# Kernel optimization log

Hardware: AMD Instinct MI355X
Metric: run time of the kernel (lower is better)

The kernel has to match this reference:

```python
import jax, jax.numpy as jnp
import numpy as np

B, P, D, H = 4, 2048, 768, 12
DFF = 4 * D
EPS = 1e-3  # Keras LayerNormalization default epsilon
SURVIVAL_PROB = 0.9  # inference-mode droppath scaling


def setup_inputs() -> dict:
    key = jax.random.key(0)
    ks = jax.random.split(key, 4)
    s = 0.02
    return {
        "x": jax.random.normal(ks[0], (B, P, D), dtype=jnp.float32),
        "ln1_g": jnp.ones((D,), jnp.float32),
        "ln1_b": jnp.zeros((D,), jnp.float32),
        "w_qkv": jax.random.normal(ks[1], (D, 3 * D), jnp.float32) * s,
        "b_qkv": jnp.zeros((3 * D,), jnp.float32),
        "ln2_g": jnp.ones((D,), jnp.float32),
        "ln2_b": jnp.zeros((D,), jnp.float32),
        "w1": jax.random.normal(ks[2], (D, DFF), jnp.float32) * s,
        "b1": jnp.zeros((DFF,), jnp.float32),
        "w2": jax.random.normal(ks[3], (DFF, D), jnp.float32) * s,
        "b2": jnp.zeros((D,), jnp.float32),
    }


def _layernorm(x, g, b):
    mu = jnp.mean(x, axis=-1, keepdims=True)
    var = jnp.mean(jnp.square(x - mu), axis=-1, keepdims=True)
    return (x - mu) * jax.lax.rsqrt(var + EPS) * g + b


def _block(x, ln1_g, ln1_b, w_qkv, b_qkv, ln2_g, ln2_b, w1, b1, w2, b2):
    # --- pre-norm self-attention ---
    h = _layernorm(x, ln1_g, ln1_b)
    qkv = h @ w_qkv + b_qkv                      # [B,P,3D]
    q, k, v = jnp.split(qkv, 3, axis=-1)
    hd = D // H
    to_heads = lambda t: t.reshape(B, P, H, hd).transpose(0, 2, 1, 3)  # b h p c
    q, k, v = to_heads(q), to_heads(k), to_heads(v)
    scale = jnp.sqrt(jnp.float32(D / H))
    scores = jnp.einsum('bhqc,bhkc->bhqk', q, k) / scale
    attn = jax.nn.softmax(scores, axis=-1)
    o = jnp.einsum('bhqk,bhkc->bhqc', attn, v)
    o = o.transpose(0, 2, 1, 3).reshape(B, P, D)
    x = o * SURVIVAL_PROB + x
    # --- pre-norm MLP ---
    h = _layernorm(x, ln2_g, ln2_b)
    h = jax.nn.gelu(h @ w1 + b1, approximate=False)
    h = h @ w2 + b2
    return h * SURVIVAL_PROB + x


def reference(x, ln1_g, ln1_b, w_qkv, b_qkv, ln2_g, ln2_b, w1, b1, w2, b2):
    return _block(x, ln1_g, ln1_b, w_qkv, b_qkv, ln2_g, ln2_b, w1, b1, w2, b2)
```

## Files before the change

kernel.cpp:

```cpp
#include <hip/hip_runtime.h>
#include <hip/hip_bf16.h>
#include <math.h>

#define B_ 4
#define P_ 2048
#define D_ 768
#define H_ 12

typedef __attribute__((ext_vector_type(8))) short bf16x8;
typedef __attribute__((ext_vector_type(4))) float f32x4;

static __device__ __forceinline__ short f2bf(float f) {
  union { float f; unsigned u; } z; z.f = f;
  unsigned r = z.u + 0x7fffu + ((z.u >> 16) & 1u);
  return (short)(r >> 16);
}

static __device__ __forceinline__ float bf2f(short s) {
  union { unsigned u; float f; } z;
  z.u = ((unsigned)(unsigned short)s) << 16;
  return z.f;
}

static __device__ __forceinline__ void gll16(const void* g, void* l) {
  __builtin_amdgcn_global_load_lds(
      (const __attribute__((address_space(1))) void*)g,
      (__attribute__((address_space(3))) void*)l, 16, 0, 0);
}

static __device__ __forceinline__ int vswz(int d) {
  return ((d & 7) ^ ((d >> 3) & 7)) << 3;
}

__global__ __launch_bounds__(256) void tcvt_kernel(const float* __restrict__ in,
                                                   short* __restrict__ out, int K, int N) {
  __shared__ float t[32][33];
  int k0 = blockIdx.x * 32, n0 = blockIdx.y * 32;
  int tx = threadIdx.x & 31, ty = threadIdx.x >> 5;
#pragma unroll
  for (int i = 0; i < 4; ++i)
    t[ty + 8 * i][tx] = in[(size_t)(k0 + ty + 8 * i) * N + n0 + tx];
  __syncthreads();
#pragma unroll
  for (int i = 0; i < 4; ++i)
    out[(size_t)(n0 + ty + 8 * i) * K + k0 + tx] = f2bf(t[tx][ty + 8 * i]);
}

__global__ __launch_bounds__(256) void ln_kernel(const float* __restrict__ in,
                                                 const float* __restrict__ g,
                                                 const float* __restrict__ be,
                                                 short* __restrict__ out) {
  int row = blockIdx.x, tid = threadIdx.x;
  const float* xr = in + (size_t)row * D_;
  float v0 = xr[tid], v1 = xr[tid + 256], v2 = xr[tid + 512];
  float s = v0 + v1 + v2;
  float ss = v0 * v0 + v1 * v1 + v2 * v2;
#pragma unroll
  for (int d = 1; d < 64; d <<= 1) {
    s += __shfl_xor(s, d, 64);
    ss += __shfl_xor(ss, d, 64);
  }
  __shared__ float red[8];
  int w = tid >> 6;
  if ((tid & 63) == 0) { red[w] = s; red[4 + w] = ss; }
  __syncthreads();
  s = red[0] + red[1] + red[2] + red[3];
  ss = red[4] + red[5] + red[6] + red[7];
  float mu = s * (1.0f / D_);
  float rstd = rsqrtf(ss * (1.0f / D_) - mu * mu + 1e-3f);
  short* orow = out + (size_t)row * D_;
  orow[tid]       = f2bf((v0 - mu) * rstd * g[tid]       + be[tid]);
  orow[tid + 256] = f2bf((v1 - mu) * rstd * g[tid + 256] + be[tid + 256]);
  orow[tid + 512] = f2bf((v2 - mu) * rstd * g[tid + 512] + be[tid + 512]);
}

template <int EPI>
__global__ __launch_bounds__(256, 3) void gemm128(
    const short* __restrict__ A, const short* __restrict__ Bt,
    const float* __restrict__ bias, short* __restrict__ out_bf,
    float* __restrict__ out_f, const float* __restrict__ resid,
    int M, int N, int K) {
  alignas(16) __shared__ short a_lds[2][128 * 32];
  alignas(16) __shared__ short b_lds[2][128 * 32];
  const int tid = threadIdx.x;
  const int wv = tid >> 6, lane = tid & 63;
  const int wm = wv >> 1, wn = wv & 1;
  const int g = lane >> 4, r = lane & 15;
  const int m0 = blockIdx.x * 128, n0 = blockIdx.y * 128;
  const int srow = lane >> 2, sseg = lane & 3;
  f32x4 acc[4][4] = {};
  const short* aptr = A + (size_t)(m0 + wv * 16 + srow) * K + sseg * 8;
  const short* bptr = Bt + (size_t)(n0 + wv * 16 + srow) * K + sseg * 8;
  const int aoff = (wv * 16) * 32;

  gll16(aptr, &a_lds[0][aoff]);
  gll16(aptr + (size_t)64 * K, &a_lds[0][aoff + 64 * 32]);
  gll16(bptr, &b_lds[0][aoff]);
  gll16(bptr + (size_t)64 * K, &b_lds[0][aoff + 64 * 32]);
  __syncthreads();

  const int nt = K / 32;
  int cur = 0;
  for (int t = 0; t < nt; ++t) {
    if (t + 1 < nt) {
      const int k0 = (t + 1) * 32;
      const int nb = cur ^ 1;
      gll16(aptr + k0, &a_lds[nb][aoff]);
      gll16(aptr + k0 + (size_t)64 * K, &a_lds[nb][aoff + 64 * 32]);
      gll16(bptr + k0, &b_lds[nb][aoff]);
      gll16(bptr + k0 + (size_t)64 * K, &b_lds[nb][aoff + 64 * 32]);
    }
    bf16x8 af[4], bfr[4];
#pragma unroll
    for (int i = 0; i < 4; ++i)
      af[i] = *reinterpret_cast<const bf16x8*>(&a_lds[cur][(wm * 64 + i * 16 + r) * 32 + g * 8]);
#pragma unroll
    for (int i = 0; i < 4; ++i)
      bfr[i] = *reinterpret_cast<const bf16x8*>(&b_lds[cur][(wn * 64 + i * 16 + r) * 32 + g * 8]);
#pragma unroll
    for (int i = 0; i < 4; ++i)
#pragma unroll
      for (int jn = 0; jn < 4; ++jn)
        acc[i][jn] = __builtin_amdgcn_mfma_f32_16x16x32_bf16(af[i], bfr[jn], acc[i][jn], 0, 0, 0);
    __syncthreads();
    cur ^= 1;
  }
#pragma unroll
  for (int i = 0; i < 4; ++i) {
#pragma unroll
    for (int jn = 0; jn < 4; ++jn) {
      int col = n0 + wn * 64 + jn * 16 + r;
      float bb = bias[col];
#pragma unroll
      for (int jj = 0; jj < 4; ++jj) {
        int row = m0 + wm * 64 + i * 16 + g * 4 + jj;
        float v = acc[i][jn][jj] + bb;
        size_t idx = (size_t)row * N + col;
        if (EPI == 0) {
          out_bf[idx] = f2bf(v);
        } else if (EPI == 1) {
          v = 0.5f * v * (1.0f + erff(v * 0.70710678118654752f));
          out_bf[idx] = f2bf(v);
        } else {
          out_f[idx] = v * 0.9f + resid[idx];
        }
      }
    }
  }
}

__global__ __launch_bounds__(256, 3) void attn_kernel(const short* __restrict__ qkv,
                                                      const float* __restrict__ x,
                                                      float* __restrict__ x2) {
  alignas(16) __shared__ short k_lds[64 * 72];
  alignas(16) __shared__ short vt_lds[64 * 64];
  alignas(16) __shared__ short p_lds[4][32 * 72];
  const int tid = threadIdx.x, wv = tid >> 6, lane = tid & 63;
  const int g = lane >> 4, r = lane & 15;
  const int b = blockIdx.y / H_, h = blockIdx.y % H_;
  const int TD = 3 * D_;
  const int qrow0 = blockIdx.x * 128 + wv * 32;
  bf16x8 qf[2][2];
#pragma unroll
  for (int mf = 0; mf < 2; ++mf)
#pragma unroll
    for (int kb = 0; kb < 2; ++kb) {
      bf16x8 q = *reinterpret_cast<const bf16x8*>(
          qkv + (size_t)(b * P_ + qrow0 + mf * 16 + r) * TD + h * 64 + kb * 32 + g * 8);
#pragma unroll
      for (int e = 0; e < 8; ++e) q[e] = f2bf(bf2f(q[e]) * 0.125f);
      qf[mf][kb] = q;
    }
  f32x4 acc[2][4] = {};
  float m_run[2], l_run[2];
#pragma unroll
  for (int mf = 0; mf < 2; ++mf) { m_run[mf] = -1e30f; l_run[mf] = 0.0f; }
  const int lrow = tid >> 2, lseg = tid & 3;
  short* p_w = &p_lds[wv][0];
  const int bcast = 20 * g;
  for (int kc = 0; kc < P_; kc += 64) {
    const short* src = qkv + (size_t)(b * P_ + kc + lrow) * TD + D_ + h * 64 + lseg * 16;
    bf16x8 kv0 = *reinterpret_cast<const bf16x8*>(src);
    bf16x8 kv1 = *reinterpret_cast<const bf16x8*>(src + 8);
    bf16x8 vv0 = *reinterpret_cast<const bf16x8*>(src + D_);
    bf16x8 vv1 = *reinterpret_cast<const bf16x8*>(src + D_ + 8);
    __syncthreads();
    *reinterpret_cast<bf16x8*>(&k_lds[lrow * 72 + lseg * 16]) = kv0;
    *reinterpret_cast<bf16x8*>(&k_lds[lrow * 72 + lseg * 16 + 8]) = kv1;
#pragma unroll
    for (int j = 0; j < 8; ++j) {
      int d0 = lseg * 16 + j, d1 = d0 + 8;
      vt_lds[d0 * 64 + (lrow ^ vswz(d0))] = vv0[j];
      vt_lds[d1 * 64 + (lrow ^ vswz(d1))] = vv1[j];
    }
    __syncthreads();
    f32x4 st[2][4];
#pragma unroll
    for (int cf = 0; cf < 4; ++cf) {
      bf16x8 kf0 = *reinterpret_cast<const bf16x8*>(&k_lds[(cf * 16 + r) * 72 + g * 8]);
      bf16x8 kf1 = *reinterpret_cast<const bf16x8*>(&k_lds[(cf * 16 + r) * 72 + 32 + g * 8]);
#pragma unroll
      for (int mf = 0; mf < 2; ++mf) {
        f32x4 s = {};
        s = __builtin_amdgcn_mfma_f32_16x16x32_bf16(kf0, qf[mf][0], s, 0, 0, 0);
        s = __builtin_amdgcn_mfma_f32_16x16x32_bf16(kf1, qf[mf][1], s, 0, 0, 0);
        st[mf][cf] = s;
      }
    }
#pragma unroll
    for (int mf = 0; mf < 2; ++mf) {
      float mx = st[mf][0][0];
#pragma unroll
      for (int cf = 0; cf < 4; ++cf)
#pragma unroll
        for (int j = 0; j < 4; ++j) mx = fmaxf(mx, st[mf][cf][j]);
      mx = fmaxf(mx, __shfl_xor(mx, 16, 64));
      mx = fmaxf(mx, __shfl_xor(mx, 32, 64));
      if (!__all(mx - m_run[mf] <= 8.0f)) {
        float mn = fmaxf(m_run[mf], mx);
        float corr = __expf(m_run[mf] - mn);
        m_run[mf] = mn;
        l_run[mf] *= corr;
        float cb0 = __shfl(corr, bcast + 0, 64);
        float cb1 = __shfl(corr, bcast + 1, 64);
        float cb2 = __shfl(corr, bcast + 2, 64);
        float cb3 = __shfl(corr, bcast + 3, 64);
#pragma unroll
        for (int cf = 0; cf < 4; ++cf) {
          acc[mf][cf][0] *= cb0; acc[mf][cf][1] *= cb1;
          acc[mf][cf][2] *= cb2; acc[mf][cf][3] *= cb3;
        }
      }
      float mn = m_run[mf];
      float p[4][4];
      float ls = 0.0f;
#pragma unroll
      for (int cf = 0; cf < 4; ++cf)
#pragma unroll
        for (int j = 0; j < 4; ++j) {
          float pv = __expf(st[mf][cf][j] - mn);
          p[cf][j] = pv;
          ls += pv;
        }
      ls += __shfl_xor(ls, 16, 64);
      ls += __shfl_xor(ls, 32, 64);
      l_run[mf] += ls;
      short* prow = &p_w[(mf * 16 + r) * 72];
#pragma unroll
      for (int cf = 0; cf < 4; ++cf) {
        __hip_bfloat162 lo = __float22bfloat162_rn(make_float2(p[cf][0], p[cf][1]));
        __hip_bfloat162 hi = __float22bfloat162_rn(make_float2(p[cf][2], p[cf][3]));
        union { __hip_bfloat162 h2; unsigned u; } c0, c1;
        c0.h2 = lo; c1.h2 = hi;
        *reinterpret_cast<uint2*>(&prow[cf * 16 + 4 * g]) = make_uint2(c0.u, c1.u);
      }
    }
    bf16x8 vf[4][2];
#pragma unroll
    for (int cf = 0; cf < 4; ++cf) {
      int d = cf * 16 + r;
      int sw = vswz(d);
      vf[cf][0] = *reinterpret_cast<const bf16x8*>(&vt_lds[d * 64 + ((g * 8) ^ sw)]);
      vf[cf][1] = *reinterpret_cast<const bf16x8*>(&vt_lds[d * 64 + ((32 + g * 8) ^ sw)]);
    }
#pragma unroll
    for (int mf = 0; mf < 2; ++mf) {
      bf16x8 pf0 = *reinterpret_cast<const bf16x8*>(&p_w[(mf * 16 + r) * 72 + g * 8]);
      bf16x8 pf1 = *reinterpret_cast<const bf16x8*>(&p_w[(mf * 16 + r) * 72 + 32 + g * 8]);
#pragma unroll
      for (int cf = 0; cf < 4; ++cf) {
        acc[mf][cf] = __builtin_amdgcn_mfma_f32_16x16x32_bf16(pf0, vf[cf][0], acc[mf][cf], 0, 0, 0);
        acc[mf][cf] = __builtin_amdgcn_mfma_f32_16x16x32_bf16(pf1, vf[cf][1], acc[mf][cf], 0, 0, 0);
      }
    }
  }
#pragma unroll
  for (int mf = 0; mf < 2; ++mf) {
    float lb0 = 0.9f / __shfl(l_run[mf], bcast + 0, 64);
    float lb1 = 0.9f / __shfl(l_run[mf], bcast + 1, 64);
    float lb2 = 0.9f / __shfl(l_run[mf], bcast + 2, 64);
    float lb3 = 0.9f / __shfl(l_run[mf], bcast + 3, 64);
    float lb[4] = {lb0, lb1, lb2, lb3};
#pragma unroll
    for (int cf = 0; cf < 4; ++cf) {
      int col = h * 64 + cf * 16 + r;
#pragma unroll
      for (int j = 0; j < 4; ++j) {
        int row = qrow0 + mf * 16 + g * 4 + j;
        size_t idx = (size_t)(b * P_ + row) * D_ + col;
        x2[idx] = acc[mf][cf][j] * lb[j] + x[idx];
      }
    }
  }
}

extern "C" void kernel_launch(void* const* d_in, const int* in_sizes, int n_in,
                              void* d_out, int out_size, void* d_ws, size_t ws_size,
                              hipStream_t stream) {
  const float* x     = (const float*)d_in[0];
  const float* ln1_g = (const float*)d_in[1];
  const float* ln1_b = (const float*)d_in[2];
  const float* w_qkv = (const float*)d_in[3];
  const float* b_qkv = (const float*)d_in[4];
  const float* ln2_g = (const float*)d_in[5];
  const float* ln2_b = (const float*)d_in[6];
  const float* w1    = (const float*)d_in[7];
  const float* b1    = (const float*)d_in[8];
  const float* w2    = (const float*)d_in[9];
  const float* b2    = (const float*)d_in[10];
  float* out = (float*)d_out;
  char* ws = (char*)d_ws;

  short* wqkv_t = (short*)(ws);
  short* w1_t   = (short*)(ws + 3538944);
  short* w2_t   = (short*)(ws + 8257536);
  short* h_bf   = (short*)(ws + 12976128);
  short* qkv_bf = (short*)(ws + 25559040);
  short* a1_bf  = qkv_bf;

  const int R = B_ * P_;

  { dim3 g2(768 / 32, 2304 / 32);  tcvt_kernel<<<g2, 256, 0, stream>>>(w_qkv, wqkv_t, 768, 2304); }
  { dim3 g2(768 / 32, 3072 / 32);  tcvt_kernel<<<g2, 256, 0, stream>>>(w1, w1_t, 768, 3072); }
  { dim3 g2(3072 / 32, 768 / 32);  tcvt_kernel<<<g2, 256, 0, stream>>>(w2, w2_t, 3072, 768); }

  ln_kernel<<<R, 256, 0, stream>>>(x, ln1_g, ln1_b, h_bf);

  {
    dim3 grid(R / 128, 2304 / 128);
    gemm128<0><<<grid, 256, 0, stream>>>(h_bf, wqkv_t, b_qkv, qkv_bf, nullptr, nullptr,
                                         R, 2304, 768);
  }
  {
    dim3 grid(P_ / 128, B_ * H_);
    attn_kernel<<<grid, 256, 0, stream>>>(qkv_bf, x, out);
  }
  ln_kernel<<<R, 256, 0, stream>>>(out, ln2_g, ln2_b, h_bf);
  {
    dim3 grid(R / 128, 3072 / 128);
    gemm128<1><<<grid, 256, 0, stream>>>(h_bf, w1_t, b1, a1_bf, nullptr, nullptr,
                                         R, 3072, 768);
  }
  {
    dim3 grid(R / 128, 768 / 128);
    gemm128<2><<<grid, 256, 0, stream>>>(a1_bf, w2_t, b2, nullptr, out, out,
                                         R, 768, 3072);
  }
}
```

Before: 400.3 us.

## Widen attention KV tiles to 128, prefetch next tile into registers, swizzle GEMM LDS

```diff
diff --git a/kernel.cpp b/kernel.cpp
--- a/kernel.cpp
+++ b/kernel.cpp
@@ -26,10 +26,6 @@
   __builtin_amdgcn_global_load_lds(
       (const __attribute__((address_space(1))) void*)g,
       (__attribute__((address_space(3))) void*)l, 16, 0, 0);
-}
-
-static __device__ __forceinline__ int vswz(int d) {
-  return ((d & 7) ^ ((d >> 3) & 7)) << 3;
 }
 
 __global__ __launch_bounds__(256) void tcvt_kernel(const float* __restrict__ in,
@@ -89,8 +85,9 @@
   const int m0 = blockIdx.x * 128, n0 = blockIdx.y * 128;
   const int srow = lane >> 2, sseg = lane & 3;
   f32x4 acc[4][4] = {};
-  const short* aptr = A + (size_t)(m0 + wv * 16 + srow) * K + sseg * 8;
-  const short* bptr = Bt + (size_t)(n0 + wv * 16 + srow) * K + sseg * 8;
+  const int sw_seg = sseg ^ (srow & 3);
+  const short* aptr = A + (size_t)(m0 + wv * 16 + srow) * K + sw_seg * 8;
+  const short* bptr = Bt + (size_t)(n0 + wv * 16 + srow) * K + sw_seg * 8;
   const int aoff = (wv * 16) * 32;
 
   gll16(aptr, &a_lds[0][aoff]);
@@ -113,10 +110,12 @@
     bf16x8 af[4], bfr[4];
 #pragma unroll
     for (int i = 0; i < 4; ++i)
-      af[i] = *reinterpret_cast<const bf16x8*>(&a_lds[cur][(wm * 64 + i * 16 + r) * 32 + g * 8]);
+      af[i] = *reinterpret_cast<const bf16x8*>(
+          &a_lds[cur][(wm * 64 + i * 16 + r) * 32 + ((g ^ (r & 3)) * 8)]);
 #pragma unroll
     for (int i = 0; i < 4; ++i)
-      bfr[i] = *reinterpret_cast<const bf16x8*>(&b_lds[cur][(wn * 64 + i * 16 + r) * 32 + g * 8]);
+      bfr[i] = *reinterpret_cast<const bf16x8*>(
+          &b_lds[cur][(wn * 64 + i * 16 + r) * 32 + ((g ^ (r & 3)) * 8)]);
 #pragma unroll
     for (int i = 0; i < 4; ++i)
 #pragma unroll
@@ -149,12 +148,12 @@
   }
 }
 
-__global__ __launch_bounds__(256, 3) void attn_kernel(const short* __restrict__ qkv,
+__global__ __launch_bounds__(256, 2) void attn_kernel(const short* __restrict__ qkv,
                                                       const float* __restrict__ x,
                                                       float* __restrict__ x2) {
-  alignas(16) __shared__ short k_lds[64 * 72];
-  alignas(16) __shared__ short vt_lds[64 * 64];
-  alignas(16) __shared__ short p_lds[4][32 * 72];
+  alignas(16) __shared__ short k_lds[128 * 64];
+  alignas(16) __shared__ short vt_lds[64 * 128];
+  alignas(16) __shared__ short p_lds[4][32 * 128];
   const int tid = threadIdx.x, wv = tid >> 6, lane = tid & 63;
   const int g = lane >> 4, r = lane & 15;
   const int b = blockIdx.y / H_, h = blockIdx.y % H_;
@@ -175,30 +174,45 @@
   float m_run[2], l_run[2];
 #pragma unroll
   for (int mf = 0; mf < 2; ++mf) { m_run[mf] = -1e30f; l_run[mf] = 0.0f; }
-  const int lrow = tid >> 2, lseg = tid & 3;
-  short* p_w = &p_lds[wv][0];
+
+  const int krow = tid >> 1, dhalf = tid & 1;
+  const short* kv0src = qkv + (size_t)(b * P_ + krow) * TD + D_ + h * 64 + dhalf * 32;
+  char* p_w = (char*)&p_lds[wv][0];
   const int bcast = 20 * g;
-  for (int kc = 0; kc < P_; kc += 64) {
-    const short* src = qkv + (size_t)(b * P_ + kc + lrow) * TD + D_ + h * 64 + lseg * 16;
-    bf16x8 kv0 = *reinterpret_cast<const bf16x8*>(src);
-    bf16x8 kv1 = *reinterpret_cast<const bf16x8*>(src + 8);
-    bf16x8 vv0 = *reinterpret_cast<const bf16x8*>(src + D_);
-    bf16x8 vv1 = *reinterpret_cast<const bf16x8*>(src + D_ + 8);
+  const int rsw = (r & 7) << 4;
+
+  bf16x8 kreg[4], vreg[4];
+#pragma unroll
+  for (int c = 0; c < 4; ++c) {
+    kreg[c] = *reinterpret_cast<const bf16x8*>(kv0src + c * 8);
+    vreg[c] = *reinterpret_cast<const bf16x8*>(kv0src + D_ + c * 8);
+  }
+
+  for (int kc = 0; kc < P_; kc += 128) {
     __syncthreads();
-    *reinterpret_cast<bf16x8*>(&k_lds[lrow * 72 + lseg * 16]) = kv0;
-    *reinterpret_cast<bf16x8*>(&k_lds[lrow * 72 + lseg * 16 + 8]) = kv1;
-#pragma unroll
-    for (int j = 0; j < 8; ++j) {
-      int d0 = lseg * 16 + j, d1 = d0 + 8;
-      vt_lds[d0 * 64 + (lrow ^ vswz(d0))] = vv0[j];
-      vt_lds[d1 * 64 + (lrow ^ vswz(d1))] = vv1[j];
+    {
+      char* kb_ = (char*)&k_lds[krow * 64];
+      const int ksw = (krow & 7) << 4;
+#pragma unroll
+      for (int c = 0; c < 4; ++c)
+        *reinterpret_cast<bf16x8*>(kb_ + ((dhalf * 64 + c * 16) ^ ksw)) = kreg[c];
+#pragma unroll
+      for (int c = 0; c < 4; ++c)
+#pragma unroll
+        for (int j = 0; j < 8; ++j) {
+          int d = dhalf * 32 + c * 8 + j;
+          *reinterpret_cast<short*>((char*)vt_lds + d * 256 + ((krow * 2) ^ ((d & 7) << 4))) =
+              vreg[c][j];
+        }
     }
     __syncthreads();
-    f32x4 st[2][4];
-#pragma unroll
-    for (int cf = 0; cf < 4; ++cf) {
-      bf16x8 kf0 = *reinterpret_cast<const bf16x8*>(&k_lds[(cf * 16 + r) * 72 + g * 8]);
-      bf16x8 kf1 = *reinterpret_cast<const bf16x8*>(&k_lds[(cf * 16 + r) * 72 + 32 + g * 8]);
+    f32x4 st[2][8];
+#pragma unroll
+    for (int cf = 0; cf < 8; ++cf) {
+      int row = cf * 16 + r;
+      const char* kb_ = (const char*)k_lds + row * 128;
+      bf16x8 kf0 = *reinterpret_cast<const bf16x8*>(kb_ + ((g * 16) ^ rsw));
+      bf16x8 kf1 = *reinterpret_cast<const bf16x8*>(kb_ + ((64 + g * 16) ^ rsw));
 #pragma unroll
       for (int mf = 0; mf < 2; ++mf) {
         f32x4 s = {};
@@ -207,11 +221,19 @@
         st[mf][cf] = s;
       }
     }
+    if (kc + 128 < P_) {
+      const short* src = kv0src + (size_t)(kc + 128) * TD;
+#pragma unroll
+      for (int c = 0; c < 4; ++c) {
+        kreg[c] = *reinterpret_cast<const bf16x8*>(src + c * 8);
+        vreg[c] = *reinterpret_cast<const bf16x8*>(src + D_ + c * 8);
+      }
+    }
 #pragma unroll
     for (int mf = 0; mf < 2; ++mf) {
       float mx = st[mf][0][0];
 #pragma unroll
-      for (int cf = 0; cf < 4; ++cf)
+      for (int cf = 0; cf < 8; ++cf)
 #pragma unroll
         for (int j = 0; j < 4; ++j) mx = fmaxf(mx, st[mf][cf][j]);
       mx = fmaxf(mx, __shfl_xor(mx, 16, 64));
@@ -232,45 +254,43 @@
         }
       }
       float mn = m_run[mf];
-      float p[4][4];
       float ls = 0.0f;
-#pragma unroll
-      for (int cf = 0; cf < 4; ++cf)
-#pragma unroll
-        for (int j = 0; j < 4; ++j) {
-          float pv = __expf(st[mf][cf][j] - mn);
-          p[cf][j] = pv;
-          ls += pv;
-        }
+      char* prow = p_w + (mf * 16 + r) * 256;
+#pragma unroll
+      for (int cf = 0; cf < 8; ++cf) {
+        float p0 = __expf(st[mf][cf][0] - mn);
+        float p1 = __expf(st[mf][cf][1] - mn);
+        float p2 = __expf(st[mf][cf][2] - mn);
+        float p3 = __expf(st[mf][cf][3] - mn);
+        ls += (p0 + p1) + (p2 + p3);
+        __hip_bfloat162 lo = __float22bfloat162_rn(make_float2(p0, p1));
+        __hip_bfloat162 hi = __float22bfloat162_rn(make_float2(p2, p3));
+        union { __hip_bfloat162 h2; unsigned u; } c0, c1;
+        c0.h2 = lo; c1.h2 = hi;
+        *reinterpret_cast<uint2*>(prow + ((cf * 32 + 8 * g) ^ rsw)) = make_uint2(c0.u, c1.u);
+      }
       ls += __shfl_xor(ls, 16, 64);
       ls += __shfl_xor(ls, 32, 64);
       l_run[mf] += ls;
-      short* prow = &p_w[(mf * 16 + r) * 72];
-#pragma unroll
-      for (int cf = 0; cf < 4; ++cf) {
-        __hip_bfloat162 lo = __float22bfloat162_rn(make_float2(p[cf][0], p[cf][1]));
-        __hip_bfloat162 hi = __float22bfloat162_rn(make_float2(p[cf][2], p[cf][3]));
-        union { __hip_bfloat162 h2; unsigned u; } c0, c1;
-        c0.h2 = lo; c1.h2 = hi;
-        *reinterpret_cast<uint2*>(&prow[cf * 16 + 4 * g]) = make_uint2(c0.u, c1.u);
-      }
-    }
-    bf16x8 vf[4][2];
+    }
+    bf16x8 vf[4][4];
 #pragma unroll
     for (int cf = 0; cf < 4; ++cf) {
       int d = cf * 16 + r;
-      int sw = vswz(d);
-      vf[cf][0] = *reinterpret_cast<const bf16x8*>(&vt_lds[d * 64 + ((g * 8) ^ sw)]);
-      vf[cf][1] = *reinterpret_cast<const bf16x8*>(&vt_lds[d * 64 + ((32 + g * 8) ^ sw)]);
+      const char* vb = (const char*)vt_lds + d * 256;
+#pragma unroll
+      for (int ks = 0; ks < 4; ++ks)
+        vf[cf][ks] = *reinterpret_cast<const bf16x8*>(vb + ((ks * 64 + g * 16) ^ rsw));
     }
 #pragma unroll
     for (int mf = 0; mf < 2; ++mf) {
-      bf16x8 pf0 = *reinterpret_cast<const bf16x8*>(&p_w[(mf * 16 + r) * 72 + g * 8]);
-      bf16x8 pf1 = *reinterpret_cast<const bf16x8*>(&p_w[(mf * 16 + r) * 72 + 32 + g * 8]);
-#pragma unroll
-      for (int cf = 0; cf < 4; ++cf) {
-        acc[mf][cf] = __builtin_amdgcn_mfma_f32_16x16x32_bf16(pf0, vf[cf][0], acc[mf][cf], 0, 0, 0);
-        acc[mf][cf] = __builtin_amdgcn_mfma_f32_16x16x32_bf16(pf1, vf[cf][1], acc[mf][cf], 0, 0, 0);
+      const char* prow = p_w + (mf * 16 + r) * 256;
+#pragma unroll
+      for (int ks = 0; ks < 4; ++ks) {
+        bf16x8 pf = *reinterpret_cast<const bf16x8*>(prow + ((ks * 64 + g * 16) ^ rsw));
+#pragma unroll
+        for (int cf = 0; cf < 4; ++cf)
+          acc[mf][cf] = __builtin_amdgcn_mfma_f32_16x16x32_bf16(pf, vf[cf][ks], acc[mf][cf], 0, 0, 0);
       }
     }
   }
```

New measurement: 394.8 us. Within noise of the previous version (-1.4%).
